# Performance work log

Measured on AMD Instinct MI355X. Metric: run time of the kernel, lower is better.

The kernel has to match this reference:

```python
import jax, jax.numpy as jnp
import numpy as np

B = 1024        # batch of independent network evaluations
N_IN = 1024     # num_inputs
L = 5           # topological layers
NPL = 2048      # nodes per layer
FANIN = 16      # fixed fan-in per node
N_OUT = 256     # num_outputs (last 256 nodes of last layer)


def setup_inputs() -> dict:
    key = jax.random.key(0)
    k_in, k_src, k_w, k_b = jax.random.split(key, 4)
    inputs = jax.random.normal(k_in, (B, N_IN), dtype=jnp.float32)
    # edge sources for layer l must point at previously-evaluated nodes (< N_IN + l*NPL)
    src_layers = []
    for l in range(L):
        kl = jax.random.fold_in(k_src, l)
        hi = N_IN + l * NPL
        src_layers.append(jax.random.randint(kl, (NPL, FANIN), 0, hi, dtype=jnp.int32))
    edge_src = jnp.stack(src_layers)                                   # [L, NPL, FANIN]
    edge_w = jax.random.normal(k_w, (L, NPL, FANIN), dtype=jnp.float32) * 0.1
    biases = jax.random.normal(k_b, (L, NPL), dtype=jnp.float32) * 0.1
    return {"inputs": inputs, "edge_src": edge_src, "edge_w": edge_w, "biases": biases}


def reference(inputs, edge_src, edge_w, biases):
    # vals holds node values in topological/evaluation order: [B, n_nodes_so_far]
    vals = inputs
    for l in range(L):
        gathered = vals[:, edge_src[l]]                                # [B, NPL, FANIN] irregular gather
        node_sum = jnp.einsum('bnf,nf->bn', gathered, edge_w[l]) + biases[l]
        act = jax.nn.sigmoid if l == L - 1 else jnp.tanh               # per-node activation dispatch
        vals = jnp.concatenate([vals, act(node_sum)], axis=1)
    return vals[:, -N_OUT:]                                            # output node values
```

## Files before the change

kernel.cpp:

```cpp
#include <hip/hip_runtime.h>
#include <hip/hip_fp16.h>

#define BSZ     1024
#define N_IN    1024
#define NLAYERS 5
#define NPL     2048
#define FANIN   16
#define N_OUT   256

#define VALS_ROWS   (N_IN + 4 * NPL)
#define CPB         4
#define NBLK        (BSZ / CPB)
#define ROW_B       8
#define LDS_BYTES   (VALS_ROWS * ROW_B)

union H4 { unsigned long long u; __half2 h2[2]; };

__global__ __launch_bounds__(256) void pack_edges_kernel(
    const int* __restrict__ src, const float* __restrict__ wsrc,
    unsigned int* __restrict__ packed)
{
    int t = blockIdx.x * 256 + threadIdx.x;
    if (t >= NLAYERS * NPL) return;
    const int l = t / NPL;
    const int n = t - l * NPL;
    const int*   s  = src  + (size_t)t * FANIN;
    const float* ww = wsrc + (size_t)t * FANIN;

    int          key[FANIN];
    unsigned int val[FANIN];
#pragma unroll
    for (int f = 0; f < FANIN; ++f) {
        unsigned int idx = (unsigned int)s[f];
        key[f] = (int)(idx & 15u);
        unsigned int hi = (l < NLAYERS - 1) ? (idx << 3)
                                            : idx;
        unsigned short hw = __half_as_ushort(__float2half(ww[f]));
        val[f] = (hi << 16) | (unsigned int)hw;
    }

    unsigned int* dst = packed + (size_t)t * FANIN;
#pragma unroll
    for (int f = 0; f < FANIN; ++f) {
        int rank = 0;
#pragma unroll
        for (int g = 0; g < FANIN; ++g)
            rank += (key[g] < key[f]) || (key[g] == key[f] && g < f);
        dst[(rank - n) & 15] = val[f];
    }
}

__device__ __forceinline__ float fast_tanh(float x) {
    float t = __expf(2.0f * x);
    return 1.0f - 2.0f / (t + 1.0f);
}
__device__ __forceinline__ float fast_sigmoid(float x) {
    return 1.0f / (1.0f + __expf(-x));
}

__global__ __launch_bounds__(1024) void fused_net_kernel(
    const float* __restrict__ inputs,
    const unsigned int* __restrict__ packed,
    const float* __restrict__ biases,
    float* __restrict__ out)
{
    extern __shared__ char lds[];
    const int tid = threadIdx.x;
    const int c0  = blockIdx.x * CPB;

    {
        float v0 = inputs[(size_t)(c0 + 0) * N_IN + tid];
        float v1 = inputs[(size_t)(c0 + 1) * N_IN + tid];
        float v2 = inputs[(size_t)(c0 + 2) * N_IN + tid];
        float v3 = inputs[(size_t)(c0 + 3) * N_IN + tid];
        H4 rec;
        rec.h2[0] = __halves2half2(__float2half(v0), __float2half(v1));
        rec.h2[1] = __halves2half2(__float2half(v2), __float2half(v3));
        *reinterpret_cast<unsigned long long*>(lds + (size_t)tid * ROW_B) = rec.u;
    }
    __syncthreads();

    unsigned int pkA[FANIN], pkB[FANIN];

#pragma unroll
    for (int f = 0; f < FANIN; ++f)
        pkA[f] = packed[(size_t)tid * FANIN + f];

    for (int l = 0; l < NLAYERS - 1; ++l) {
        const float* bl = biases + (size_t)l * NPL;
        const int wbase = N_IN + l * NPL;

#pragma unroll
        for (int f = 0; f < FANIN; ++f)
            pkB[f] = packed[((size_t)l * NPL + 1024 + tid) * FANIN + f];

        {
            const int n = tid;
            const float bv = bl[n];
            float a0 = bv, a1 = bv, a2 = bv, a3 = bv;
#pragma unroll
            for (int f = 0; f < FANIN; ++f) {
                const unsigned int u   = pkA[f];
                const unsigned int off = u >> 16;
                H4 v;
                v.u = *reinterpret_cast<const unsigned long long*>(lds + off);
                const float wf = __half2float(
                    __ushort_as_half((unsigned short)(u & 0xffffu)));
                a0 = fmaf(__half2float(v.h2[0].x), wf, a0);
                a1 = fmaf(__half2float(v.h2[0].y), wf, a1);
                a2 = fmaf(__half2float(v.h2[1].x), wf, a2);
                a3 = fmaf(__half2float(v.h2[1].y), wf, a3);
            }
            a0 = fast_tanh(a0); a1 = fast_tanh(a1);
            a2 = fast_tanh(a2); a3 = fast_tanh(a3);
            H4 rec;
            rec.h2[0] = __halves2half2(__float2half(a0), __float2half(a1));
            rec.h2[1] = __halves2half2(__float2half(a2), __float2half(a3));
            *reinterpret_cast<unsigned long long*>(
                lds + (size_t)(wbase + n) * ROW_B) = rec.u;
        }

        if (l < NLAYERS - 2) {
#pragma unroll
            for (int f = 0; f < FANIN; ++f)
                pkA[f] = packed[((size_t)(l + 1) * NPL + tid) * FANIN + f];
        } else if (tid < N_OUT) {
            const int n4 = NPL - N_OUT + tid;
#pragma unroll
            for (int f = 0; f < FANIN; ++f)
                pkA[f] = packed[((size_t)(NLAYERS - 1) * NPL + n4) * FANIN + f];
        }

        {
            const int n = 1024 + tid;
            const float bv = bl[n];
            float a0 = bv, a1 = bv, a2 = bv, a3 = bv;
#pragma unroll
            for (int f = 0; f < FANIN; ++f) {
                const unsigned int u   = pkB[f];
                const unsigned int off = u >> 16;
                H4 v;
                v.u = *reinterpret_cast<const unsigned long long*>(lds + off);
                const float wf = __half2float(
                    __ushort_as_half((unsigned short)(u & 0xffffu)));
                a0 = fmaf(__half2float(v.h2[0].x), wf, a0);
                a1 = fmaf(__half2float(v.h2[0].y), wf, a1);
                a2 = fmaf(__half2float(v.h2[1].x), wf, a2);
                a3 = fmaf(__half2float(v.h2[1].y), wf, a3);
            }
            a0 = fast_tanh(a0); a1 = fast_tanh(a1);
            a2 = fast_tanh(a2); a3 = fast_tanh(a3);
            H4 rec;
            rec.h2[0] = __halves2half2(__float2half(a0), __float2half(a1));
            rec.h2[1] = __halves2half2(__float2half(a2), __float2half(a3));
            *reinterpret_cast<unsigned long long*>(
                lds + (size_t)(wbase + n) * ROW_B) = rec.u;
        }
        __syncthreads();
    }

    if (tid < N_OUT) {
        const int n = NPL - N_OUT + tid;
        const float bv = biases[(size_t)(NLAYERS - 1) * NPL + n];
        float a0 = bv, a1 = bv, a2 = bv, a3 = bv;
#pragma unroll
        for (int f = 0; f < FANIN; ++f) {
            const unsigned int u   = pkA[f];
            const unsigned int off = (u >> 16) << 3;
            H4 v;
            v.u = *reinterpret_cast<const unsigned long long*>(lds + off);
            const float wf = __half2float(
                __ushort_as_half((unsigned short)(u & 0xffffu)));
            a0 = fmaf(__half2float(v.h2[0].x), wf, a0);
            a1 = fmaf(__half2float(v.h2[0].y), wf, a1);
            a2 = fmaf(__half2float(v.h2[1].x), wf, a2);
            a3 = fmaf(__half2float(v.h2[1].y), wf, a3);
        }
        a0 = fast_sigmoid(a0); a1 = fast_sigmoid(a1);
        a2 = fast_sigmoid(a2); a3 = fast_sigmoid(a3);
        const int j = tid;
        out[(size_t)(c0 + 0) * N_OUT + j] = a0;
        out[(size_t)(c0 + 1) * N_OUT + j] = a1;
        out[(size_t)(c0 + 2) * N_OUT + j] = a2;
        out[(size_t)(c0 + 3) * N_OUT + j] = a3;
    }
}

extern "C" void kernel_launch(void* const* d_in, const int* in_sizes, int n_in,
                              void* d_out, int out_size, void* d_ws, size_t ws_size,
                              hipStream_t stream)
{
    const float* inputs   = (const float*)d_in[0];
    const int*   edge_src = (const int*)  d_in[1];
    const float* edge_w   = (const float*)d_in[2];
    const float* biases   = (const float*)d_in[3];
    float* out = (float*)d_out;
    unsigned int* packed = (unsigned int*)d_ws;

    pack_edges_kernel<<<(NLAYERS * NPL + 255) / 256, 256, 0, stream>>>(
        edge_src, edge_w, packed);

    fused_net_kernel<<<NBLK, 1024, LDS_BYTES, stream>>>(
        inputs, packed, biases, out);
}
```

Before: 25.97 us.

## Prune layer-3 nodes unused by outputs via prefix-scan compaction

```diff
diff --git a/kernel.cpp b/kernel.cpp
--- a/kernel.cpp
+++ b/kernel.cpp
@@ -13,42 +13,16 @@
 #define NBLK        (BSZ / CPB)
 #define ROW_B       8
 #define LDS_BYTES   (VALS_ROWS * ROW_B)
+#define L3_BASE     (N_IN + 3 * NPL)
+
+#define PK012_OFF   0
+#define PK3C_OFF    98304
+#define PK4_OFF     131072
+#define LIST3_OFF   135168
+#define CNT3_OFF    137216
+#define BIAS3C_OFF  137248
 
 union H4 { unsigned long long u; __half2 h2[2]; };
-
-__global__ __launch_bounds__(256) void pack_edges_kernel(
-    const int* __restrict__ src, const float* __restrict__ wsrc,
-    unsigned int* __restrict__ packed)
-{
-    int t = blockIdx.x * 256 + threadIdx.x;
-    if (t >= NLAYERS * NPL) return;
-    const int l = t / NPL;
-    const int n = t - l * NPL;
-    const int*   s  = src  + (size_t)t * FANIN;
-    const float* ww = wsrc + (size_t)t * FANIN;
-
-    int          key[FANIN];
-    unsigned int val[FANIN];
-#pragma unroll
-    for (int f = 0; f < FANIN; ++f) {
-        unsigned int idx = (unsigned int)s[f];
-        key[f] = (int)(idx & 15u);
-        unsigned int hi = (l < NLAYERS - 1) ? (idx << 3)
-                                            : idx;
-        unsigned short hw = __half_as_ushort(__float2half(ww[f]));
-        val[f] = (hi << 16) | (unsigned int)hw;
-    }
-
-    unsigned int* dst = packed + (size_t)t * FANIN;
-#pragma unroll
-    for (int f = 0; f < FANIN; ++f) {
-        int rank = 0;
-#pragma unroll
-        for (int g = 0; g < FANIN; ++g)
-            rank += (key[g] < key[f]) || (key[g] == key[f] && g < f);
-        dst[(rank - n) & 15] = val[f];
-    }
-}
 
 __device__ __forceinline__ float fast_tanh(float x) {
     float t = __expf(2.0f * x);
@@ -58,15 +32,125 @@
     return 1.0f / (1.0f + __expf(-x));
 }
 
+__global__ __launch_bounds__(1024) void prep_kernel(
+    const int* __restrict__ src, const float* __restrict__ wsrc,
+    const float* __restrict__ biases, unsigned int* __restrict__ ws)
+{
+    const int tid = threadIdx.x;
+
+    if (blockIdx.x < 24) {
+        if (tid >= 256) return;
+        const int t = blockIdx.x * 256 + tid;
+        const int n = t & (NPL - 1);
+        const int*   s  = src  + (size_t)t * FANIN;
+        const float* ww = wsrc + (size_t)t * FANIN;
+
+        int          key[FANIN];
+        unsigned int val[FANIN];
+#pragma unroll
+        for (int f = 0; f < FANIN; ++f) {
+            unsigned int idx = (unsigned int)s[f];
+            key[f] = (int)(idx & 15u);
+            unsigned short hw = __half_as_ushort(__float2half(ww[f]));
+            val[f] = ((idx << 3) << 16) | (unsigned int)hw;
+        }
+        unsigned int* dst = ws + PK012_OFF + (size_t)t * FANIN;
+#pragma unroll
+        for (int f = 0; f < FANIN; ++f) {
+            int rank = 0;
+#pragma unroll
+            for (int g = 0; g < FANIN; ++g)
+                rank += (key[g] < key[f]) || (key[g] == key[f] && g < f);
+            dst[(rank - n) & 15] = val[f];
+        }
+        return;
+    }
+
+    __shared__ unsigned int bufA[NPL];
+    __shared__ unsigned int bufB[NPL];
+    bufA[tid] = 0u; bufA[tid + 1024] = 0u;
+    __syncthreads();
+
+    const int base4 = (4 * NPL + (NPL - N_OUT)) * FANIN;
+#pragma unroll
+    for (int e = tid; e < N_OUT * FANIN; e += 1024) {
+        unsigned int idx = (unsigned int)src[base4 + e];
+        unsigned short hw = __half_as_ushort(__float2half(wsrc[base4 + e]));
+        ws[PK4_OFF + e] = (idx << 16) | (unsigned int)hw;
+        if (idx >= (unsigned)L3_BASE) bufA[idx - L3_BASE] = 1u;
+    }
+    __syncthreads();
+
+    unsigned int* a = bufA;
+    unsigned int* b = bufB;
+    for (int d = 1; d < NPL; d <<= 1) {
+        for (int i = tid; i < NPL; i += 1024)
+            b[i] = a[i] + (i >= d ? a[i - d] : 0u);
+        __syncthreads();
+        unsigned int* t2 = a; a = b; b = t2;
+    }
+    const unsigned int total = a[NPL - 1];
+    if (tid == 0) ws[CNT3_OFF] = total;
+
+    for (int j = tid; j < NPL; j += 1024) {
+        const unsigned int inc  = a[j];
+        const unsigned int prev = j ? a[j - 1] : 0u;
+        if (inc > prev) {
+            const int i = (int)inc - 1;
+            ws[LIST3_OFF + i] = (unsigned int)j;
+            ((float*)ws)[BIAS3C_OFF + i] = biases[(size_t)3 * NPL + j];
+            const int t3 = (3 * NPL + j) * FANIN;
+#pragma unroll
+            for (int f = 0; f < FANIN; ++f) {
+                unsigned int idx = (unsigned int)src[t3 + f];
+                unsigned short hw = __half_as_ushort(__float2half(wsrc[t3 + f]));
+                ws[PK3C_OFF + (size_t)i * FANIN + ((f + i) & 15)] =
+                    ((idx << 3) << 16) | (unsigned int)hw;
+            }
+        }
+    }
+}
+
+__device__ __forceinline__ void node_tanh(
+    const unsigned int* pk, float bv, int row, char* lds)
+{
+    float a0 = bv, a1 = bv, a2 = bv, a3 = bv;
+#pragma unroll
+    for (int f = 0; f < FANIN; ++f) {
+        const unsigned int u   = pk[f];
+        const unsigned int off = u >> 16;
+        H4 v;
+        v.u = *reinterpret_cast<const unsigned long long*>(lds + off);
+        const float wf = __half2float(
+            __ushort_as_half((unsigned short)(u & 0xffffu)));
+        a0 = fmaf(__half2float(v.h2[0].x), wf, a0);
+        a1 = fmaf(__half2float(v.h2[0].y), wf, a1);
+        a2 = fmaf(__half2float(v.h2[1].x), wf, a2);
+        a3 = fmaf(__half2float(v.h2[1].y), wf, a3);
+    }
+    a0 = fast_tanh(a0); a1 = fast_tanh(a1);
+    a2 = fast_tanh(a2); a3 = fast_tanh(a3);
+    H4 rec;
+    rec.h2[0] = __halves2half2(__float2half(a0), __float2half(a1));
+    rec.h2[1] = __halves2half2(__float2half(a2), __float2half(a3));
+    *reinterpret_cast<unsigned long long*>(lds + (size_t)row * ROW_B) = rec.u;
+}
+
 __global__ __launch_bounds__(1024) void fused_net_kernel(
     const float* __restrict__ inputs,
-    const unsigned int* __restrict__ packed,
+    const unsigned int* __restrict__ ws,
     const float* __restrict__ biases,
     float* __restrict__ out)
 {
     extern __shared__ char lds[];
     const int tid = threadIdx.x;
     const int c0  = blockIdx.x * CPB;
+    const unsigned int* pk012 = ws + PK012_OFF;
+    const unsigned int* pk3c  = ws + PK3C_OFF;
+    const unsigned int* pk4   = ws + PK4_OFF;
+    const unsigned int* list3 = ws + LIST3_OFF;
+    const float* bias3c = (const float*)(ws + BIAS3C_OFF);
+    const int cnt3 = (int)ws[CNT3_OFF];
 
     {
         float v0 = inputs[(size_t)(c0 + 0) * N_IN + tid];
@@ -81,87 +165,63 @@
     __syncthreads();
 
     unsigned int pkA[FANIN], pkB[FANIN];
+    int   n3a = 0, n3b = 0;
+    float b3a = 0.f, b3b = 0.f;
 
 #pragma unroll
     for (int f = 0; f < FANIN; ++f)
-        pkA[f] = packed[(size_t)tid * FANIN + f];
-
-    for (int l = 0; l < NLAYERS - 1; ++l) {
+        pkA[f] = pk012[(size_t)tid * FANIN + f];
+
+    for (int l = 0; l < 3; ++l) {
         const float* bl = biases + (size_t)l * NPL;
         const int wbase = N_IN + l * NPL;
 
 #pragma unroll
         for (int f = 0; f < FANIN; ++f)
-            pkB[f] = packed[((size_t)l * NPL + 1024 + tid) * FANIN + f];
-
-        {
-            const int n = tid;
-            const float bv = bl[n];
-            float a0 = bv, a1 = bv, a2 = bv, a3 = bv;
-#pragma unroll
-            for (int f = 0; f < FANIN; ++f) {
-                const unsigned int u   = pkA[f];
-                const unsigned int off = u >> 16;
-                H4 v;
-                v.u = *reinterpret_cast<const unsigned long long*>(lds + off);
-                const float wf = __half2float(
-                    __ushort_as_half((unsigned short)(u & 0xffffu)));
-                a0 = fmaf(__half2float(v.h2[0].x), wf, a0);
-                a1 = fmaf(__half2float(v.h2[0].y), wf, a1);
-                a2 = fmaf(__half2float(v.h2[1].x), wf, a2);
-                a3 = fmaf(__half2float(v.h2[1].y), wf, a3);
-            }
-            a0 = fast_tanh(a0); a1 = fast_tanh(a1);
-            a2 = fast_tanh(a2); a3 = fast_tanh(a3);
-            H4 rec;
-            rec.h2[0] = __halves2half2(__float2half(a0), __float2half(a1));
-            rec.h2[1] = __halves2half2(__float2half(a2), __float2half(a3));
-            *reinterpret_cast<unsigned long long*>(
-                lds + (size_t)(wbase + n) * ROW_B) = rec.u;
-        }
-
-        if (l < NLAYERS - 2) {
-#pragma unroll
-            for (int f = 0; f < FANIN; ++f)
-                pkA[f] = packed[((size_t)(l + 1) * NPL + tid) * FANIN + f];
-        } else if (tid < N_OUT) {
-            const int n4 = NPL - N_OUT + tid;
-#pragma unroll
-            for (int f = 0; f < FANIN; ++f)
-                pkA[f] = packed[((size_t)(NLAYERS - 1) * NPL + n4) * FANIN + f];
-        }
-
-        {
-            const int n = 1024 + tid;
-            const float bv = bl[n];
-            float a0 = bv, a1 = bv, a2 = bv, a3 = bv;
-#pragma unroll
-            for (int f = 0; f < FANIN; ++f) {
-                const unsigned int u   = pkB[f];
-                const unsigned int off = u >> 16;
-                H4 v;
-                v.u = *reinterpret_cast<const unsigned long long*>(lds + off);
-                const float wf = __half2float(
-                    __ushort_as_half((unsigned short)(u & 0xffffu)));
-                a0 = fmaf(__half2float(v.h2[0].x), wf, a0);
-                a1 = fmaf(__half2float(v.h2[0].y), wf, a1);
-                a2 = fmaf(__half2float(v.h2[1].x), wf, a2);
-                a3 = fmaf(__half2float(v.h2[1].y), wf, a3);
-            }
-            a0 = fast_tanh(a0); a1 = fast_tanh(a1);
-            a2 = fast_tanh(a2); a3 = fast_tanh(a3);
-            H4 rec;
-            rec.h2[0] = __halves2half2(__float2half(a0), __float2half(a1));
-            rec.h2[1] = __halves2half2(__float2half(a2), __float2half(a3));
-            *reinterpret_cast<unsigned long long*>(
-                lds + (size_t)(wbase + n) * ROW_B) = rec.u;
-        }
+            pkB[f] = pk012[((size_t)l * NPL + 1024 + tid) * FANIN + f];
+
+        node_tanh(pkA, bl[tid], wbase + tid, lds);
+
+        if (l < 2) {
+#pragma unroll
+            for (int f = 0; f < FANIN; ++f)
+                pkA[f] = pk012[((size_t)(l + 1) * NPL + tid) * FANIN + f];
+        } else if (tid < cnt3) {
+            n3a = (int)list3[tid];
+            b3a = bias3c[tid];
+#pragma unroll
+            for (int f = 0; f < FANIN; ++f)
+                pkA[f] = pk3c[(size_t)tid * FANIN + f];
+        }
+
+        node_tanh(pkB, bl[1024 + tid], wbase + 1024 + tid, lds);
         __syncthreads();
     }
 
+    {
+        const int i1 = 1024 + tid;
+        if (i1 < cnt3) {
+            n3b = (int)list3[i1];
+            b3b = bias3c[i1];
+#pragma unroll
+            for (int f = 0; f < FANIN; ++f)
+                pkB[f] = pk3c[(size_t)i1 * FANIN + f];
+        }
+        if (tid < cnt3)
+            node_tanh(pkA, b3a, L3_BASE + n3a, lds);
+
+        if (tid < N_OUT) {
+#pragma unroll
+            for (int f = 0; f < FANIN; ++f)
+                pkA[f] = pk4[(size_t)tid * FANIN + f];
+        }
+        if (i1 < cnt3)
+            node_tanh(pkB, b3b, L3_BASE + n3b, lds);
+        __syncthreads();
+    }
+
     if (tid < N_OUT) {
-        const int n = NPL - N_OUT + tid;
-        const float bv = biases[(size_t)(NLAYERS - 1) * NPL + n];
+        const float bv = biases[(size_t)4 * NPL + (NPL - N_OUT) + tid];
         float a0 = bv, a1 = bv, a2 = bv, a3 = bv;
 #pragma unroll
         for (int f = 0; f < FANIN; ++f) {
@@ -195,11 +255,10 @@
     const float* edge_w   = (const float*)d_in[2];
     const float* biases   = (const float*)d_in[3];
     float* out = (float*)d_out;
-    unsigned int* packed = (unsigned int*)d_ws;
-
-    pack_edges_kernel<<<(NLAYERS * NPL + 255) / 256, 256, 0, stream>>>(
-        edge_src, edge_w, packed);
+    unsigned int* ws = (unsigned int*)d_ws;
+
+    prep_kernel<<<25, 1024, 0, stream>>>(edge_src, edge_w, biases, ws);
 
     fused_net_kernel<<<NBLK, 1024, LDS_BYTES, stream>>>(
-        inputs, packed, biases, out);
-}
+        inputs, ws, biases, out);
+}
```

Result: slower. 34.56 us (+33.1%).
